# Kernel optimization log

Measured on AMD Instinct MI355X. Metric: run time of the kernel, lower is better.

Reference implementation:

```python
import jax, jax.numpy as jnp
import numpy as np

H, KVH, D, HID = 32, 32, 128, 4096
THETA = 10000.0
EPS = 1e-5


def setup_inputs() -> dict:
    key = jax.random.key(0)
    ks = jax.random.split(key, 7)
    T = 2048
    return {
        "positions": jnp.arange(T, dtype=jnp.int32),
        "hidden_states": jax.random.normal(ks[0], (T, HID), dtype=jnp.float32),
        "w_qkv": jax.random.normal(ks[1], ((H + 2 * KVH) * D, HID), dtype=jnp.float32) * 0.02,
        "w_o": jax.random.normal(ks[2], (HID, H * D), dtype=jnp.float32) * 0.02,
        "q_norm_w": jax.random.uniform(ks[3], (H, D), dtype=jnp.float32),
        "q_norm_b": jax.random.normal(ks[4], (H, D), dtype=jnp.float32) * 0.02,
        "k_norm_w": jax.random.uniform(ks[5], (KVH, D), dtype=jnp.float32),
        "k_norm_b": jax.random.normal(ks[6], (KVH, D), dtype=jnp.float32) * 0.02,
    }


def _per_head_ln(x, w, b):
    # x: [T, H, D]; layer_norm over last dim without affine, then *w + b (per head)
    mu = jnp.mean(x, axis=-1, keepdims=True)
    var = jnp.mean(jnp.square(x - mu), axis=-1, keepdims=True)
    xn = (x - mu) * jax.lax.rsqrt(var + EPS)
    return xn * w + b


def _rope(x, positions):
    # neox-style rotate-half RoPE; x: [T, H, D]
    half = D // 2
    inv_freq = 1.0 / (THETA ** (jnp.arange(0, D, 2, dtype=jnp.float32) / D))  # [D/2]
    freqs = positions.astype(jnp.float32)[:, None] * inv_freq  # [T, D/2]
    cos = jnp.cos(freqs)[:, None, :]  # [T, 1, D/2]
    sin = jnp.sin(freqs)[:, None, :]
    x1, x2 = x[..., :half], x[..., half:]
    return jnp.concatenate([x1 * cos - x2 * sin, x2 * cos + x1 * sin], axis=-1)


def reference(positions, hidden_states, w_qkv, w_o, q_norm_w, q_norm_b, k_norm_w, k_norm_b):
    T = hidden_states.shape[0]
    qkv = hidden_states @ w_qkv.T  # [T, (H+2*KVH)*D]
    q, k, v = jnp.split(qkv, [H * D, (H + KVH) * D], axis=-1)
    q = q.reshape(T, H, D)
    k = k.reshape(T, KVH, D)
    v = v.reshape(T, KVH, D)
    q = _per_head_ln(q, q_norm_w, q_norm_b)
    k = _per_head_ln(k, k_norm_w, k_norm_b)
    q = _rope(q, positions)
    k = _rope(k, positions)
    scale = D ** -0.5
    scores = jnp.einsum("qhd,khd->hqk", q, k) * scale  # [H, T, T]
    causal = jnp.tril(jnp.ones((T, T), dtype=bool))
    scores = jnp.where(causal, scores, jnp.finfo(scores.dtype).min)
    probs = jax.nn.softmax(scores, axis=-1)
    attn = jnp.einsum("hqk,khd->qhd", probs, v).reshape(T, H * D)
    return attn @ w_o.T  # [T, HID]
```

## Files before the change

### kernel.cpp

```cpp
#include <hip/hip_runtime.h>
#include <cstdint>

typedef unsigned short u16;
typedef __attribute__((ext_vector_type(8))) __bf16 bf16x8;
typedef __attribute__((ext_vector_type(4))) float f32x4;

__device__ __forceinline__ u16 f2bf(float f) {
  unsigned int u = __builtin_bit_cast(unsigned int, f);
  unsigned int r = (u + 0x7fffu + ((u >> 16) & 1u)) >> 16;
  return (u16)r;
}

__device__ __forceinline__ void gload16(const u16* g, u16* l) {
  __builtin_amdgcn_global_load_lds((const __attribute__((address_space(1))) void*)g,
                                   (__attribute__((address_space(3))) void*)l, 16, 0, 0);
}

__device__ __forceinline__ int swz64i(int row, int col) {
  return row * 64 + (((col & 0x38) ^ ((row & 7) << 3)) | (col & 7));
}
__device__ __forceinline__ int swz128i(int row, int col) {
  return row * 128 + (((col & 0x78) ^ ((row & 7) << 3)) | (col & 7));
}

__global__ __launch_bounds__(256) void cvt_bf16_kernel(const float* __restrict__ in,
                                                       u16* __restrict__ out, long n4) {
  long i = (long)blockIdx.x * 256 + threadIdx.x;
  long stride = (long)gridDim.x * 256;
  const float4* in4 = (const float4*)in;
  uint2* out2 = (uint2*)out;
  for (long k = i; k < n4; k += stride) {
    float4 v = in4[k];
    uint2 o;
    o.x = (unsigned int)f2bf(v.x) | ((unsigned int)f2bf(v.y) << 16);
    o.y = (unsigned int)f2bf(v.z) | ((unsigned int)f2bf(v.w) << 16);
    out2[k] = o;
  }
}

__global__ __launch_bounds__(512, 2) void gemm192(const u16* __restrict__ A,
                                                  const u16* __restrict__ B,
                                                  float* __restrict__ C,
                                                  int Ndim, int Kdim) {
  extern __shared__ __align__(16) u16 lds[];
  const int tid = threadIdx.x;
  const int lane = tid & 63, wave = tid >> 6;
  const int wr = wave >> 2, wc = wave & 3;
  const int l15 = lane & 15, l4 = lane >> 4;
  const int gx = gridDim.x;
  int lin = blockIdx.y * gx + blockIdx.x;
  const int xcd = lin & 7, ii = lin >> 3;
  const int bx = xcd * (gx >> 3) + (ii >> 3), by = ii & 7;
  const long arow = (long)by * 256, brow = (long)bx * 192;
  const int NT = Kdim >> 6;

  const int rowt = tid >> 3;
  const int koff = ((tid & 7) ^ (rowt & 7)) * 8;
  const u16* gA[4];
  const u16* gB[3];
  #pragma unroll
  for (int r = 0; r < 4; ++r) gA[r] = A + (size_t)(arow + rowt + r * 64) * Kdim + koff;
  #pragma unroll
  for (int r = 0; r < 3; ++r) gB[r] = B + (size_t)(brow + rowt + r * 64) * Kdim + koff;
  u16* const ldsB = lds + 32768;

  auto STA = [&](int u) {
    u16* d = lds + (u & 1) * 16384 + tid * 8;
    #pragma unroll
    for (int r = 0; r < 4; ++r) gload16(gA[r] + (size_t)u * 64, d + r * 4096);
  };
  auto STB = [&](int u) {
    u16* d = ldsB + (u & 1) * 12288 + tid * 8;
    #pragma unroll
    for (int r = 0; r < 3; ++r) gload16(gB[r] + (size_t)u * 64, d + r * 4096);
  };

  bf16x8 af[8][2], bfr[2];
  f32x4 acc[8][3] = {};
  int cks[2];
  #pragma unroll
  for (int kc = 0; kc < 2; ++kc) cks[kc] = (((kc * 4 + l4) ^ (l15 & 7)) * 8);

  auto LDA = [&](int u) {
    const u16* base = lds + (u & 1) * 16384 + (wr * 128 + l15) * 64;
    #pragma unroll
    for (int m = 0; m < 8; ++m)
      #pragma unroll
      for (int kc = 0; kc < 2; ++kc)
        af[m][kc] = *(const bf16x8*)(base + m * 1024 + cks[kc]);
  };
  auto LDB = [&](int u, int nh) {
    const u16* base = ldsB + (u & 1) * 12288 + (wc * 48 + nh * 16 + l15) * 64;
    #pragma unroll
    for (int kc = 0; kc < 2; ++kc)
      bfr[kc] = *(const bf16x8*)(base + cks[kc]);
  };
  auto MMQ = [&](int nh) {
    #pragma unroll
    for (int kc = 0; kc < 2; ++kc)
      #pragma unroll
      for (int m = 0; m < 8; ++m)
        acc[m][nh] = __builtin_amdgcn_mfma_f32_16x16x32_bf16(af[m][kc], bfr[kc],
                                                             acc[m][nh], 0, 0, 0);
  };

#define PH_BEGIN() do { __builtin_amdgcn_s_barrier();                         \
    asm volatile("s_waitcnt lgkmcnt(0)" ::: "memory");                        \
    __builtin_amdgcn_sched_barrier(0);                                        \
    __builtin_amdgcn_s_setprio(1); } while (0)
#define PH_END() do { __builtin_amdgcn_s_setprio(0);                          \
    __builtin_amdgcn_s_barrier(); } while (0)

  STA(0); STB(0); STA(1);
  asm volatile("s_waitcnt vmcnt(4)" ::: "memory");
  __builtin_amdgcn_s_barrier();

  for (int u = 0; u < NT; ++u) {
    LDA(u); LDB(u, 0);
    if (u + 1 < NT) STB(u + 1);
    PH_BEGIN(); MMQ(0); PH_END();
    LDB(u, 1);
    if (u + 2 < NT) STA(u + 2);
    PH_BEGIN(); MMQ(1); PH_END();
    LDB(u, 2);
    PH_BEGIN(); MMQ(2);
    __builtin_amdgcn_s_setprio(0);
    if (u + 2 < NT) { asm volatile("s_waitcnt vmcnt(4)" ::: "memory"); }
    else            { asm volatile("s_waitcnt vmcnt(0)" ::: "memory"); }
    __builtin_amdgcn_s_barrier();
  }
#undef PH_BEGIN
#undef PH_END

  #pragma unroll
  for (int m = 0; m < 8; ++m)
    #pragma unroll
    for (int nh = 0; nh < 3; ++nh)
      #pragma unroll
      for (int j = 0; j < 4; ++j) {
        long r = arow + wr * 128 + m * 16 + l4 * 4 + j;
        long c = brow + wc * 48 + nh * 16 + l15;
        C[r * Ndim + c] = acc[m][nh][j];
      }
}

__global__ __launch_bounds__(512, 2) void gemm256(const u16* __restrict__ A,
                                                  const u16* __restrict__ B,
                                                  float* __restrict__ C,
                                                  int Ndim, int Kdim) {
  extern __shared__ __align__(16) u16 lds[];
  const int tid = threadIdx.x;
  const int lane = tid & 63, wave = tid >> 6;
  const int wr = wave >> 2, wc = wave & 3;
  const int l15 = lane & 15, l4 = lane >> 4;
  const int gx = gridDim.x;
  int lin = blockIdx.y * gx + blockIdx.x;
  const int xcd = lin & 7, ii = lin >> 3;
  const int bx = xcd * (gx >> 3) + (ii >> 3), by = ii & 7;
  const long arow = (long)by * 256, brow = (long)bx * 128;
  const int NT = Kdim >> 6;

  const int rowt = tid >> 3;
  const int koff = ((tid & 7) ^ (rowt & 7)) * 8;
  const u16* gA[4];
  const u16* gB[2];
  #pragma unroll
  for (int r = 0; r < 4; ++r) gA[r] = A + (size_t)(arow + rowt + r * 64) * Kdim + koff;
  #pragma unroll
  for (int r = 0; r < 2; ++r) gB[r] = B + (size_t)(brow + rowt + r * 64) * Kdim + koff;

  auto STA = [&](int u) {
    u16* d = lds + (u % 3) * 16384 + tid * 8;
    #pragma unroll
    for (int r = 0; r < 4; ++r) gload16(gA[r] + (size_t)u * 64, d + r * 4096);
  };
  auto STB = [&](int u) {
    u16* d = lds + 49152 + (u & 1) * 8192 + tid * 8;
    #pragma unroll
    for (int r = 0; r < 2; ++r) gload16(gB[r] + (size_t)u * 64, d + r * 4096);
  };

  bf16x8 af[4][2], bfr[2][2];
  f32x4 acc[8][2] = {};
  int cks[2];
  #pragma unroll
  for (int kc = 0; kc < 2; ++kc) cks[kc] = (((kc * 4 + l4) ^ (l15 & 7)) * 8);

  auto LDA = [&](int u, int mh) {
    const u16* base = lds + (u % 3) * 16384 + (wr * 128 + mh * 64 + l15) * 64;
    #pragma unroll
    for (int m = 0; m < 4; ++m)
      #pragma unroll
      for (int kc = 0; kc < 2; ++kc)
        af[m][kc] = *(const bf16x8*)(base + m * 1024 + cks[kc]);
  };
  auto LDB = [&](int u) {
    const u16* base = lds + 49152 + (u & 1) * 8192 + (wc * 32 + l15) * 64;
    #pragma unroll
    for (int n = 0; n < 2; ++n)
      #pragma unroll
      for (int kc = 0; kc < 2; ++kc)
        bfr[n][kc] = *(const bf16x8*)(base + n * 1024 + cks[kc]);
  };
  auto MM = [&](int mh) {
    #pragma unroll
    for (int kc = 0; kc < 2; ++kc)
      #pragma unroll
      for (int m = 0; m < 4; ++m)
        #pragma unroll
        for (int n = 0; n < 2; ++n)
          acc[mh * 4 + m][n] =
            __builtin_amdgcn_mfma_f32_16x16x32_bf16(af[m][kc], bfr[n][kc],
                                                    acc[mh * 4 + m][n], 0, 0, 0);
  };

#define PH_BEGIN() do { __builtin_amdgcn_s_barrier();                         \
    asm volatile("s_waitcnt lgkmcnt(0)" ::: "memory");                        \
    __builtin_amdgcn_sched_barrier(0);                                        \
    __builtin_amdgcn_s_setprio(1); } while (0)

  STA(0); STB(0); STA(1); STB(1);
  asm volatile("s_waitcnt vmcnt(6)" ::: "memory");
  __builtin_amdgcn_s_barrier();

  for (int u = 0; u < NT; ++u) {
    LDA(u, 0); LDB(u);
    if (u + 2 < NT) STA(u + 2);
    PH_BEGIN(); MM(0);
    __builtin_amdgcn_s_setprio(0);
    __builtin_amdgcn_s_barrier();
    LDA(u, 1);
    if (u + 2 < NT) STB(u + 2);
    PH_BEGIN(); MM(1);
    __builtin_amdgcn_s_setprio(0);
    if (u + 2 < NT) { asm volatile("s_waitcnt vmcnt(6)" ::: "memory"); }
    else if (u + 1 < NT) { asm volatile("s_waitcnt vmcnt(0)" ::: "memory"); }
    __builtin_amdgcn_s_barrier();
  }
#undef PH_BEGIN

  #pragma unroll
  for (int M = 0; M < 8; ++M)
    #pragma unroll
    for (int n = 0; n < 2; ++n)
      #pragma unroll
      for (int j = 0; j < 4; ++j) {
        long r = arow + wr * 128 + M * 16 + l4 * 4 + j;
        long c = brow + wc * 32 + n * 16 + l15;
        C[r * Ndim + c] = acc[M][n][j];
      }
}

__global__ __launch_bounds__(256) void ln_rope_kernel(
    const float* __restrict__ qkv, const int* __restrict__ pos,
    const float* __restrict__ qw, const float* __restrict__ qb2,
    const float* __restrict__ kw, const float* __restrict__ kb2,
    u16* __restrict__ qo, u16* __restrict__ ko, u16* __restrict__ vo, int T) {
  const int hh = blockIdx.x;
  const int t = blockIdx.y * 4 + (threadIdx.x >> 6);
  const int lane = threadIdx.x & 63;
  const float* src = qkv + (size_t)t * 12288 + hh * 128;
  float x1 = src[lane], x2 = src[lane + 64];
  if (hh >= 64) {
    u16* dst = vo + ((size_t)(hh - 64) * T + t) * 128;
    dst[lane] = f2bf(x1); dst[lane + 64] = f2bf(x2);
    return;
  }
  float s = x1 + x2;
  #pragma unroll
  for (int off = 32; off; off >>= 1) s += __shfl_xor(s, off);
  float mu = s * (1.0f / 128.0f);
  float d1 = x1 - mu, d2 = x2 - mu;
  float vs = d1 * d1 + d2 * d2;
  #pragma unroll
  for (int off = 32; off; off >>= 1) vs += __shfl_xor(vs, off);
  float rstd = rsqrtf(vs * (1.0f / 128.0f) + 1e-5f);
  bool isq = hh < 32;
  int hl = isq ? hh : hh - 32;
  const float* w = (isq ? qw : kw) + hl * 128;
  const float* b = (isq ? qb2 : kb2) + hl * 128;
  float y1 = d1 * rstd * w[lane] + b[lane];
  float y2 = d2 * rstd * w[lane + 64] + b[lane + 64];
  float p = (float)pos[t];
  float invf = exp2f((float)lane * (-13.287712379549449f / 64.0f));
  float fr = p * invf;
  float sn, cs;
  __sincosf(fr, &sn, &cs);
  float o1 = y1 * cs - y2 * sn;
  float o2 = y2 * cs + y1 * sn;
  if (isq) {
    const float sc = 0.08838834764831845f;
    o1 *= sc; o2 *= sc;
    u16* dst = qo + ((size_t)hl * T + t) * 128;
    dst[lane] = f2bf(o1); dst[lane + 64] = f2bf(o2);
  } else {
    u16* dst = ko + ((size_t)hl * T + t) * 128;
    dst[lane] = f2bf(o1); dst[lane + 64] = f2bf(o2);
  }
}

__global__ __launch_bounds__(256, 2) void flash_kernel(
    const u16* __restrict__ qb, const u16* __restrict__ kb,
    const u16* __restrict__ vb, u16* __restrict__ attn, int T) {
  __shared__ __align__(16) u16 Ks[64 * 128];
  __shared__ __align__(16) u16 Vt[128 * 64];
  __shared__ __align__(16) u16 Ps[4][32 * 64];
  const int tid = threadIdx.x;
  const int lane = tid & 63, wave = tid >> 6;
  const int l15 = lane & 15, l4 = lane >> 4;
  const int h = blockIdx.y;
  const int qbase = blockIdx.x * 128;
  const int qrow0 = qbase + wave * 32;
  const u16* Q  = qb + (size_t)h * T * 128;
  const u16* Kp = kb + (size_t)h * T * 128;
  const u16* Vp = vb + (size_t)h * T * 128;
  const int rK0 = tid >> 4, d8k = (tid & 15) * 8;

  bf16x8 qf[2][4];
  #pragma unroll
  for (int mi = 0; mi < 2; ++mi)
    #pragma unroll
    for (int kc = 0; kc < 4; ++kc)
      qf[mi][kc] = *(const bf16x8*)&Q[(size_t)(qrow0 + mi * 16 + l15) * 128 + kc * 32 + l4 * 8];

  float m_st[2][4], l_st[2][4];
  f32x4 o[2][8] = {};
  #pragma unroll
  for (int mi = 0; mi < 2; ++mi)
    #pragma unroll
    for (int j = 0; j < 4; ++j) { m_st[mi][j] = -1e30f; l_st[mi][j] = 0.0f; }

  const int ntile = (qbase + 128) / 64;
  uint4 kr[4], vr[4];
  #pragma unroll
  for (int c = 0; c < 4; ++c) {
    kr[c] = *(const uint4*)&Kp[(size_t)(rK0 + 16 * c) * 128 + d8k];
    vr[c] = *(const uint4*)&Vp[(size_t)lane * 128 + (wave + 4 * c) * 8];
  }
  for (int kt = 0; kt < ntile; ++kt) {
    const int kbase = kt * 64;
    #pragma unroll
    for (int c = 0; c < 4; ++c) {
      *(uint4*)&Ks[swz128i(rK0 + 16 * c, d8k)] = kr[c];
      const u16* pv = (const u16*)&vr[c];
      int dv = (wave + 4 * c) * 8;
      #pragma unroll
      for (int j = 0; j < 8; ++j) Vt[swz64i(dv + j, lane)] = pv[j];
    }
    __syncthreads();
    if (kt + 1 < ntile) {
      const int nb = kbase + 64;
      #pragma unroll
      for (int c = 0; c < 4; ++c) {
        kr[c] = *(const uint4*)&Kp[(size_t)(nb + rK0 + 16 * c) * 128 + d8k];
        vr[c] = *(const uint4*)&Vp[(size_t)(nb + lane) * 128 + (wave + 4 * c) * 8];
      }
    }
    if (kbase <= qrow0 + 31) {
      f32x4 s[2][4] = {};
      __builtin_amdgcn_s_setprio(1);
      #pragma unroll
      for (int kc = 0; kc < 4; ++kc)
        #pragma unroll
        for (int nj = 0; nj < 4; ++nj) {
          bf16x8 kf = *(const bf16x8*)&Ks[swz128i(nj * 16 + l15, kc * 32 + l4 * 8)];
          #pragma unroll
          for (int mi = 0; mi < 2; ++mi)
            s[mi][nj] = __builtin_amdgcn_mfma_f32_16x16x32_bf16(qf[mi][kc], kf, s[mi][nj], 0, 0, 0);
        }
      __builtin_amdgcn_s_setprio(0);
      if (kbase + 63 > qrow0) {
        #pragma unroll
        for (int mi = 0; mi < 2; ++mi)
          #pragma unroll
          for (int nj = 0; nj < 4; ++nj)
            #pragma unroll
            for (int j = 0; j < 4; ++j) {
              int r = qrow0 + mi * 16 + l4 * 4 + j;
              int cc = kbase + nj * 16 + l15;
              if (cc > r) s[mi][nj][j] = -1e30f;
            }
      }
      float vmax[2][4];
      float dmax = -1e30f;
      #pragma unroll
      for (int mi = 0; mi < 2; ++mi)
        #pragma unroll
        for (int j = 0; j < 4; ++j) {
          float v = fmaxf(fmaxf(s[mi][0][j], s[mi][1][j]), fmaxf(s[mi][2][j], s[mi][3][j]));
          #pragma unroll
          for (int off = 1; off < 16; off <<= 1) v = fmaxf(v, __shfl_xor(v, off));
          vmax[mi][j] = v;
          dmax = fmaxf(dmax, v - m_st[mi][j]);
        }
      if (!__all(dmax <= 8.0f)) {
        #pragma unroll
        for (int mi = 0; mi < 2; ++mi)
          #pragma unroll
          for (int j = 0; j < 4; ++j) {
            float mn = fmaxf(m_st[mi][j], vmax[mi][j]);
            float scl = __expf(m_st[mi][j] - mn);
            m_st[mi][j] = mn;
            l_st[mi][j] *= scl;
            #pragma unroll
            for (int nf = 0; nf < 8; ++nf) o[mi][nf][j] *= scl;
          }
      }
      #pragma unroll
      for (int mi = 0; mi < 2; ++mi) {
        float sum[4] = {0.f, 0.f, 0.f, 0.f};
        #pragma unroll
        for (int nj = 0; nj < 4; ++nj)
          #pragma unroll
          for (int j = 0; j < 4; ++j) {
            float p = __expf(s[mi][nj][j] - m_st[mi][j]);
            s[mi][nj][j] = p;
            sum[j] += p;
          }
        #pragma unroll
        for (int j = 0; j < 4; ++j) {
          #pragma unroll
          for (int off = 1; off < 16; off <<= 1) sum[j] += __shfl_xor(sum[j], off);
          l_st[mi][j] += sum[j];
        }
        #pragma unroll
        for (int nj = 0; nj < 4; ++nj)
          #pragma unroll
          for (int j = 0; j < 4; ++j)
            Ps[wave][swz64i(mi * 16 + l4 * 4 + j, nj * 16 + l15)] = f2bf(s[mi][nj][j]);
      }
      asm volatile("s_waitcnt lgkmcnt(0)" ::: "memory");
      __builtin_amdgcn_sched_barrier(0);
      __builtin_amdgcn_s_setprio(1);
      #pragma unroll
      for (int mi = 0; mi < 2; ++mi)
        #pragma unroll
        for (int kc = 0; kc < 2; ++kc) {
          bf16x8 pf = *(const bf16x8*)&Ps[wave][swz64i(mi * 16 + l15, kc * 32 + l4 * 8)];
          #pragma unroll
          for (int nf = 0; nf < 8; ++nf) {
            bf16x8 vf = *(const bf16x8*)&Vt[swz64i(nf * 16 + l15, kc * 32 + l4 * 8)];
            o[mi][nf] = __builtin_amdgcn_mfma_f32_16x16x32_bf16(pf, vf, o[mi][nf], 0, 0, 0);
          }
        }
      __builtin_amdgcn_s_setprio(0);
    }
    __syncthreads();
  }
  #pragma unroll
  for (int mi = 0; mi < 2; ++mi) {
    float rl[4];
    #pragma unroll
    for (int j = 0; j < 4; ++j) rl[j] = 1.0f / l_st[mi][j];
    #pragma unroll
    for (int nf = 0; nf < 8; ++nf)
      #pragma unroll
      for (int j = 0; j < 4; ++j) {
        int r = qrow0 + mi * 16 + l4 * 4 + j;
        int cc = h * 128 + nf * 16 + l15;
        attn[(size_t)r * 4096 + cc] = f2bf(o[mi][nf][j] * rl[j]);
      }
  }
}

extern "C" void kernel_launch(void* const* d_in, const int* in_sizes, int n_in,
                              void* d_out, int out_size, void* d_ws, size_t ws_size,
                              hipStream_t stream) {
  const int* positions = (const int*)d_in[0];
  const float* hidden  = (const float*)d_in[1];
  const float* w_qkv   = (const float*)d_in[2];
  const float* w_o     = (const float*)d_in[3];
  const float* qnw     = (const float*)d_in[4];
  const float* qnb     = (const float*)d_in[5];
  const float* knw     = (const float*)d_in[6];
  const float* knb     = (const float*)d_in[7];
  float* out = (float*)d_out;

  const int T = in_sizes[0];
  const int HID = 4096, NQKV = 12288, H = 32;

  char* ws = (char*)d_ws;
  u16* hid_bf  = (u16*)ws;
  u16* wreg    = (u16*)(ws + (size_t)T * HID * 2);
  float* qkv_f = (float*)(ws + (size_t)T * HID * 2 + (size_t)NQKV * HID * 2);

  u16* q_bf  = wreg;
  u16* k_bf  = q_bf + (size_t)H * T * 128;
  u16* v_bf  = k_bf + (size_t)H * T * 128;
  u16* at_bf = v_bf + (size_t)H * T * 128;
  u16* wo_bf = at_bf + (size_t)T * 4096;

  hipFuncSetAttribute(reinterpret_cast<const void*>(&gemm192),
                      hipFuncAttributeMaxDynamicSharedMemorySize, 114688);
  hipFuncSetAttribute(reinterpret_cast<const void*>(&gemm256),
                      hipFuncAttributeMaxDynamicSharedMemorySize, 131072);

  cvt_bf16_kernel<<<2048, 256, 0, stream>>>(hidden, hid_bf, (long)T * HID / 4);
  cvt_bf16_kernel<<<4096, 256, 0, stream>>>(w_qkv, wreg, (long)NQKV * HID / 4);
  gemm192<<<dim3(NQKV / 192, T / 256), 512, 114688, stream>>>(hid_bf, wreg, qkv_f, NQKV, HID);
  ln_rope_kernel<<<dim3(96, T / 4), 256, 0, stream>>>(qkv_f, positions, qnw, qnb, knw, knb,
                                                      q_bf, k_bf, v_bf, T);
  cvt_bf16_kernel<<<2048, 256, 0, stream>>>(w_o, wo_bf, (long)HID * HID / 4);
  flash_kernel<<<dim3(T / 128, H), 256, 0, stream>>>(q_bf, k_bf, v_bf, at_bf, T);
  gemm256<<<dim3(HID / 128, T / 256), 512, 131072, stream>>>(at_bf, wo_bf, out, HID, HID);
}
```

Baseline: 548.1 us.

## Store QKV GEMM output as bf16 and interleave flash query rows across waves

The QKV projection now writes bf16 instead of fp32, halving the intermediate's write and read traffic; the LN/RoPE kernel reads bf16 and passes V through without conversion. Separately, flash attention reassigns query rows so each wave owns two 16-row strips spaced 64 apart, processing each strip independently with its own causal skip. This is meant to balance causal work across waves on diagonal tiles. Rounding qkv to bf16 before layernorm adds some precision loss.

```diff
diff --git a/kernel.cpp b/kernel.cpp
--- a/kernel.cpp
+++ b/kernel.cpp
@@ -9,6 +9,9 @@
   unsigned int u = __builtin_bit_cast(unsigned int, f);
   unsigned int r = (u + 0x7fffu + ((u >> 16) & 1u)) >> 16;
   return (u16)r;
+}
+__device__ __forceinline__ float bf2f(u16 u) {
+  return __builtin_bit_cast(float, (unsigned int)u << 16);
 }
 
 __device__ __forceinline__ void gload16(const u16* g, u16* l) {
@@ -40,7 +43,7 @@
 
 __global__ __launch_bounds__(512, 2) void gemm192(const u16* __restrict__ A,
                                                   const u16* __restrict__ B,
-                                                  float* __restrict__ C,
+                                                  u16* __restrict__ C,
                                                   int Ndim, int Kdim) {
   extern __shared__ __align__(16) u16 lds[];
   const int tid = threadIdx.x;
@@ -140,7 +143,7 @@
       for (int j = 0; j < 4; ++j) {
         long r = arow + wr * 128 + m * 16 + l4 * 4 + j;
         long c = brow + wc * 48 + nh * 16 + l15;
-        C[r * Ndim + c] = acc[m][nh][j];
+        C[r * Ndim + c] = f2bf(acc[m][nh][j]);
       }
 }
 
@@ -252,20 +255,21 @@
 }
 
 __global__ __launch_bounds__(256) void ln_rope_kernel(
-    const float* __restrict__ qkv, const int* __restrict__ pos,
+    const u16* __restrict__ qkv, const int* __restrict__ pos,
     const float* __restrict__ qw, const float* __restrict__ qb2,
     const float* __restrict__ kw, const float* __restrict__ kb2,
     u16* __restrict__ qo, u16* __restrict__ ko, u16* __restrict__ vo, int T) {
   const int hh = blockIdx.x;
   const int t = blockIdx.y * 4 + (threadIdx.x >> 6);
   const int lane = threadIdx.x & 63;
-  const float* src = qkv + (size_t)t * 12288 + hh * 128;
-  float x1 = src[lane], x2 = src[lane + 64];
+  const u16* src = qkv + (size_t)t * 12288 + hh * 128;
+  u16 u1 = src[lane], u2 = src[lane + 64];
   if (hh >= 64) {
     u16* dst = vo + ((size_t)(hh - 64) * T + t) * 128;
-    dst[lane] = f2bf(x1); dst[lane + 64] = f2bf(x2);
+    dst[lane] = u1; dst[lane + 64] = u2;
     return;
   }
+  float x1 = bf2f(u1), x2 = bf2f(u2);
   float s = x1 + x2;
   #pragma unroll
   for (int off = 32; off; off >>= 1) s += __shfl_xor(s, off);
@@ -310,7 +314,6 @@
   const int l15 = lane & 15, l4 = lane >> 4;
   const int h = blockIdx.y;
   const int qbase = blockIdx.x * 128;
-  const int qrow0 = qbase + wave * 32;
   const u16* Q  = qb + (size_t)h * T * 128;
   const u16* Kp = kb + (size_t)h * T * 128;
   const u16* Vp = vb + (size_t)h * T * 128;
@@ -321,7 +324,7 @@
   for (int mi = 0; mi < 2; ++mi)
     #pragma unroll
     for (int kc = 0; kc < 4; ++kc)
-      qf[mi][kc] = *(const bf16x8*)&Q[(size_t)(qrow0 + mi * 16 + l15) * 128 + kc * 32 + l4 * 8];
+      qf[mi][kc] = *(const bf16x8*)&Q[(size_t)(qbase + mi * 64 + wave * 16 + l15) * 128 + kc * 32 + l4 * 8];
 
   float m_st[2][4], l_st[2][4];
   f32x4 o[2][8] = {};
@@ -356,65 +359,58 @@
         vr[c] = *(const uint4*)&Vp[(size_t)(nb + lane) * 128 + (wave + 4 * c) * 8];
       }
     }
-    if (kbase <= qrow0 + 31) {
-      f32x4 s[2][4] = {};
-      __builtin_amdgcn_s_setprio(1);
-      #pragma unroll
-      for (int kc = 0; kc < 4; ++kc)
-        #pragma unroll
-        for (int nj = 0; nj < 4; ++nj) {
-          bf16x8 kf = *(const bf16x8*)&Ks[swz128i(nj * 16 + l15, kc * 32 + l4 * 8)];
-          #pragma unroll
-          for (int mi = 0; mi < 2; ++mi)
-            s[mi][nj] = __builtin_amdgcn_mfma_f32_16x16x32_bf16(qf[mi][kc], kf, s[mi][nj], 0, 0, 0);
-        }
-      __builtin_amdgcn_s_setprio(0);
-      if (kbase + 63 > qrow0) {
-        #pragma unroll
-        for (int mi = 0; mi < 2; ++mi)
+    #pragma unroll
+    for (int mi = 0; mi < 2; ++mi) {
+      const int r0 = qbase + mi * 64 + wave * 16;
+      if (kbase <= r0 + 15) {
+        f32x4 s[4] = {};
+        __builtin_amdgcn_s_setprio(1);
+        #pragma unroll
+        for (int kc = 0; kc < 4; ++kc)
+          #pragma unroll
+          for (int nj = 0; nj < 4; ++nj) {
+            bf16x8 kf = *(const bf16x8*)&Ks[swz128i(nj * 16 + l15, kc * 32 + l4 * 8)];
+            s[nj] = __builtin_amdgcn_mfma_f32_16x16x32_bf16(qf[mi][kc], kf, s[nj], 0, 0, 0);
+          }
+        __builtin_amdgcn_s_setprio(0);
+        if (kbase + 63 > r0) {
           #pragma unroll
           for (int nj = 0; nj < 4; ++nj)
             #pragma unroll
             for (int j = 0; j < 4; ++j) {
-              int r = qrow0 + mi * 16 + l4 * 4 + j;
+              int r = r0 + l4 * 4 + j;
               int cc = kbase + nj * 16 + l15;
-              if (cc > r) s[mi][nj][j] = -1e30f;
+              if (cc > r) s[nj][j] = -1e30f;
             }
-      }
-      float vmax[2][4];
-      float dmax = -1e30f;
-      #pragma unroll
-      for (int mi = 0; mi < 2; ++mi)
+        }
+        float vmax[4];
+        float dmax = -1e30f;
         #pragma unroll
         for (int j = 0; j < 4; ++j) {
-          float v = fmaxf(fmaxf(s[mi][0][j], s[mi][1][j]), fmaxf(s[mi][2][j], s[mi][3][j]));
+          float v = fmaxf(fmaxf(s[0][j], s[1][j]), fmaxf(s[2][j], s[3][j]));
           #pragma unroll
           for (int off = 1; off < 16; off <<= 1) v = fmaxf(v, __shfl_xor(v, off));
-          vmax[mi][j] = v;
+          vmax[j] = v;
           dmax = fmaxf(dmax, v - m_st[mi][j]);
         }
-      if (!__all(dmax <= 8.0f)) {
-        #pragma unroll
-        for (int mi = 0; mi < 2; ++mi)
+        if (!__all(dmax <= 8.0f)) {
           #pragma unroll
           for (int j = 0; j < 4; ++j) {
-            float mn = fmaxf(m_st[mi][j], vmax[mi][j]);
+            float mn = fmaxf(m_st[mi][j], vmax[j]);
             float scl = __expf(m_st[mi][j] - mn);
             m_st[mi][j] = mn;
             l_st[mi][j] *= scl;
             #pragma unroll
             for (int nf = 0; nf < 8; ++nf) o[mi][nf][j] *= scl;
           }
-      }
-      #pragma unroll
-      for (int mi = 0; mi < 2; ++mi) {
+        }
         float sum[4] = {0.f, 0.f, 0.f, 0.f};
         #pragma unroll
         for (int nj = 0; nj < 4; ++nj)
           #pragma unroll
           for (int j = 0; j < 4; ++j) {
-            float p = __expf(s[mi][nj][j] - m_st[mi][j]);
-            s[mi][nj][j] = p;
+            float p = __expf(s[nj][j] - m_st[mi][j]);
+            s[nj][j] = p;
             sum[j] += p;
           }
         #pragma unroll
@@ -427,13 +423,10 @@
         for (int nj = 0; nj < 4; ++nj)
           #pragma unroll
           for (int j = 0; j < 4; ++j)
-            Ps[wave][swz64i(mi * 16 + l4 * 4 + j, nj * 16 + l15)] = f2bf(s[mi][nj][j]);
-      }
-      asm volatile("s_waitcnt lgkmcnt(0)" ::: "memory");
-      __builtin_amdgcn_sched_barrier(0);
-      __builtin_amdgcn_s_setprio(1);
-      #pragma unroll
-      for (int mi = 0; mi < 2; ++mi)
+            Ps[wave][swz64i(mi * 16 + l4 * 4 + j, nj * 16 + l15)] = f2bf(s[nj][j]);
+        asm volatile("s_waitcnt lgkmcnt(0)" ::: "memory");
+        __builtin_amdgcn_sched_barrier(0);
+        __builtin_amdgcn_s_setprio(1);
         #pragma unroll
         for (int kc = 0; kc < 2; ++kc) {
           bf16x8 pf = *(const bf16x8*)&Ps[wave][swz64i(mi * 16 + l15, kc * 32 + l4 * 8)];
@@ -443,7 +436,8 @@
             o[mi][nf] = __builtin_amdgcn_mfma_f32_16x16x32_bf16(pf, vf, o[mi][nf], 0, 0, 0);
           }
         }
-      __builtin_amdgcn_s_setprio(0);
+        __builtin_amdgcn_s_setprio(0);
+      }
     }
     __syncthreads();
   }
@@ -456,7 +450,7 @@
     for (int nf = 0; nf < 8; ++nf)
       #pragma unroll
       for (int j = 0; j < 4; ++j) {
-        int r = qrow0 + mi * 16 + l4 * 4 + j;
+        int r = qbase + mi * 64 + wave * 16 + l4 * 4 + j;
         int cc = h * 128 + nf * 16 + l15;
         attn[(size_t)r * 4096 + cc] = f2bf(o[mi][nf][j] * rl[j]);
       }
@@ -482,7 +476,7 @@
   char* ws = (char*)d_ws;
   u16* hid_bf  = (u16*)ws;
   u16* wreg    = (u16*)(ws + (size_t)T * HID * 2);
-  float* qkv_f = (float*)(ws + (size_t)T * HID * 2 + (size_t)NQKV * HID * 2);
+  u16* qkv_bf  = (u16*)(ws + (size_t)T * HID * 2 + (size_t)NQKV * HID * 2);
 
   u16* q_bf  = wreg;
   u16* k_bf  = q_bf + (size_t)H * T * 128;
@@ -497,8 +491,8 @@
 
   cvt_bf16_kernel<<<2048, 256, 0, stream>>>(hidden, hid_bf, (long)T * HID / 4);
   cvt_bf16_kernel<<<4096, 256, 0, stream>>>(w_qkv, wreg, (long)NQKV * HID / 4);
-  gemm192<<<dim3(NQKV / 192, T / 256), 512, 114688, stream>>>(hid_bf, wreg, qkv_f, NQKV, HID);
-  ln_rope_kernel<<<dim3(96, T / 4), 256, 0, stream>>>(qkv_f, positions, qnw, qnb, knw, knb,
+  gemm192<<<dim3(NQKV / 192, T / 256), 512, 114688, stream>>>(hid_bf, wreg, qkv_bf, NQKV, HID);
+  ln_rope_kernel<<<dim3(96, T / 4), 256, 0, stream>>>(qkv_bf, positions, qnw, qnb, knw, knb,
                                                       q_bf, k_bf, v_bf, T);
   cvt_bf16_kernel<<<2048, 256, 0, stream>>>(w_o, wo_bf, (long)HID * HID / 4);
   flash_kernel<<<dim3(T / 128, H), 256, 0, stream>>>(q_bf, k_bf, v_bf, at_bf, T);
```

After: 543.9 us. No clear change (-0.8%).
